# Kernel tuning notes

Measured on AMD Instinct MI355X. Metric: run time of the kernel, lower is better.

Reference implementation:

```python
import jax, jax.numpy as jnp
import numpy as np

B, IN, H = 8192, 1024, 1024
WRANK, UR0, UR1, G = 256, 64, 32, 2
HG = H // G


def setup_inputs() -> dict:
    key = jax.random.key(0)
    ks = jax.random.split(key, 24)
    r = lambda k, shp: 0.1 * jax.random.normal(k, shp, dtype=jnp.float32)
    inp = {
        "x": jax.random.normal(ks[0], (B, IN), dtype=jnp.float32),
        "h": jax.random.normal(ks[1], (B, H), dtype=jnp.float32),
        "c": jax.random.normal(ks[2], (B, H), dtype=jnp.float32),
        "W": r(ks[3], (IN, WRANK)),
        "W1": r(ks[4], (WRANK, H)),
        "W2": r(ks[5], (WRANK, H)),
        "W3": r(ks[6], (WRANK, H)),
        "W4": r(ks[7], (WRANK, H)),
        "U": r(ks[8], (G, HG, UR0)),
        "U1": r(ks[9], (G, UR0, HG)),
        "U2": r(ks[10], (G, UR0, HG)),
        "U3": r(ks[11], (G, UR0, HG)),
        "U4": r(ks[12], (G, UR0, HG)),
        "UU": r(ks[13], (G, HG, UR1)),
        "UU1": r(ks[14], (G, UR1, HG)),
        "UU2": r(ks[15], (G, UR1, HG)),
        "UU3": r(ks[16], (G, UR1, HG)),
        "UU4": r(ks[17], (G, UR1, HG)),
        "bias_f": jnp.ones((1, H), dtype=jnp.float32),
        "bias_i": jnp.ones((1, H), dtype=jnp.float32),
        "bias_c": jnp.ones((1, H), dtype=jnp.float32),
        "bias_o": jnp.ones((1, H), dtype=jnp.float32),
    }
    return inp


def _grouped(hg, Ushare, Ui):
    # hg: [B, g, hg]; Ushare: [g, hg, r]; Ui: [g, r, hg] -> [B, H]
    t = jnp.einsum('bgd,gdr->bgr', hg, Ushare)
    return jnp.einsum('bgr,grd->bgd', t, Ui).reshape(hg.shape[0], H)


def reference(x, h, c, W, W1, W2, W3, W4, U, U1, U2, U3, U4,
              UU, UU1, UU2, UU3, UU4, bias_f, bias_i, bias_c, bias_o):
    # low-rank W path
    xw = x @ W                      # [B, wRank]
    wVal1, wVal2, wVal3, wVal4 = xw @ W1, xw @ W2, xw @ W3, xw @ W4

    # grouped low-rank U path (diagonal groups)
    hg = h.reshape(B, G, HG)
    tU = jnp.einsum('bgd,gdr->bgr', hg, U)          # shared projection
    uVal1 = jnp.einsum('bgr,grd->bgd', tU, U1).reshape(B, H)
    uVal2 = jnp.einsum('bgr,grd->bgd', tU, U2).reshape(B, H)
    uVal3 = jnp.einsum('bgr,grd->bgd', tU, U3).reshape(B, H)
    uVal4 = jnp.einsum('bgr,grd->bgd', tU, U4).reshape(B, H)

    # grouped UU path on group-rotated h (index = [1..g-1, 0])
    hg3 = jnp.roll(hg, -1, axis=1)
    tUU = jnp.einsum('bgd,gdr->bgr', hg3, UU)
    uuVal1 = jnp.einsum('bgr,grd->bgd', tUU, UU1).reshape(B, H)
    uuVal2 = jnp.einsum('bgr,grd->bgd', tUU, UU2).reshape(B, H)
    uuVal3 = jnp.einsum('bgr,grd->bgd', tUU, UU3).reshape(B, H)
    uuVal4 = jnp.einsum('bgr,grd->bgd', tUU, UU4).reshape(B, H)

    matVal_i = wVal1 + uVal1 + uuVal1
    matVal_f = wVal2 + uVal2 + uuVal2
    matVal_o = wVal3 + uVal3 + uuVal3
    matVal_c = wVal4 + uVal4 + uuVal4

    i = jax.nn.sigmoid(matVal_i + bias_i)
    f = jax.nn.sigmoid(matVal_f + bias_f)
    o = jax.nn.sigmoid(matVal_o + bias_o)
    c_tilda = jnp.tanh(matVal_c + bias_c)

    c_next = f * c + i * c_tilda
    h_next = o * jnp.tanh(c_next)
    return (c_next, h_next)
```

## Files before the change

kernel.cpp:

```cpp
#include <hip/hip_runtime.h>
#include <hip/hip_bf16.h>

#define B_ROWS 8192
#define IN_DIM 1024
#define H_DIM  1024
#define WRANK  256
#define UR0    64
#define UR1    32
#define HGD    512

#define NS2    11
#define NTA    14

typedef __attribute__((ext_vector_type(8))) short bf16x8;
typedef __attribute__((ext_vector_type(4))) float f32x4;
typedef __attribute__((ext_vector_type(4))) float float4v;

__device__ __forceinline__ unsigned short f2bf(float f) {
    union { float f; unsigned u; } v; v.f = f;
    unsigned r = v.u + 0x7FFF + ((v.u >> 16) & 1);
    return (unsigned short)(r >> 16);
}

__device__ __forceinline__ void gld16(void* lds, const void* g) {
    __builtin_amdgcn_global_load_lds(
        (const __attribute__((address_space(1))) unsigned int*)g,
        (__attribute__((address_space(3))) unsigned int*)lds, 16, 0, 0);
}

__device__ __forceinline__ float fsig(float x)  { return 1.f / (1.f + __expf(-x)); }
__device__ __forceinline__ float ftanh(float x) { return 1.f - 2.f / (__expf(2.f * x) + 1.f); }

__global__ __launch_bounds__(256)
void pack_weights(const float* __restrict__ W,
                  const float* __restrict__ W1, const float* __restrict__ W2,
                  const float* __restrict__ W3, const float* __restrict__ W4,
                  const float* __restrict__ U,  const float* __restrict__ U1,
                  const float* __restrict__ U2, const float* __restrict__ U3,
                  const float* __restrict__ U4,
                  const float* __restrict__ UU, const float* __restrict__ UU1,
                  const float* __restrict__ UU2,const float* __restrict__ UU3,
                  const float* __restrict__ UU4,
                  unsigned short* __restrict__ WbfT,
                  unsigned short* __restrict__ HPbf,
                  unsigned short* __restrict__ BT2)
{
    const float* Wg[4]  = {W1, W2, W3, W4};
    const float* Ug[4]  = {U1, U2, U3, U4};
    const float* UUg[4] = {UU1, UU2, UU3, UU4};
    const long N_WT = 256L * 1024;
    const long N_HP = 256L * 512;
    const long N_BT = 16L * NS2 * 8192;
    const long total = N_WT + N_HP + N_BT;
    for (long t = blockIdx.x * 256L + threadIdx.x; t < total; t += (long)gridDim.x * 256L) {
        if (t < N_WT) {
            int n = (int)(t >> 10), p = (int)(t & 1023);
            int span = p >> 6, slp = (p >> 3) & 7, e = p & 7;
            int k = span * 64 + ((slp ^ (n & 7)) << 3) + e;
            WbfT[t] = f2bf(W[(size_t)k * WRANK + n]);
        } else if (t < N_WT + N_HP) {
            long u = t - N_WT;
            int n = (int)(u >> 9), p = (int)(u & 511);
            int span = p >> 6, slp = (p >> 3) & 7, e = p & 7;
            int k = span * 64 + ((slp ^ (n & 7)) << 3) + e;
            float v;
            if (n < 64)       v = U [(size_t)k * UR0 + n];
            else if (n < 96)  v = UU[(size_t)(HGD + k) * UR1 + (n - 64)];
            else if (n < 128) v = 0.f;
            else if (n < 192) v = U [(size_t)(HGD + k) * UR0 + (n - 128)];
            else if (n < 224) v = UU[(size_t)k * UR1 + (n - 192)];
            else              v = 0.f;
            HPbf[u] = f2bf(v);
        } else {
            long u = t - N_WT - N_HP;
            int img = (int)(u >> 13);
            int nt = img / NS2, s = img % NS2;
            int r = (int)(u & 8191);
            int q = r >> 11, kc = (r >> 9) & 3, row = (r >> 3) & 63, e = r & 7;
            int n = nt * 64 + row, g = n >> 9, nn = n & 511;
            int kk = kc * 8 + e;
            float v;
            if (s < 8)       v = Wg[q][(size_t)(s * 32 + kk) * H_DIM + n];
            else if (s < 10) v = Ug[q][((size_t)g * UR0 + (s - 8) * 32 + kk) * HGD + nn];
            else             v = UUg[q][((size_t)g * UR1 + kk) * HGD + nn];
            BT2[u] = f2bf(v);
        }
    }
}

__global__ __launch_bounds__(256, 4)
void s1_kernel(const float* __restrict__ x, const float* __restrict__ h,
               const unsigned short* __restrict__ WbfT,
               const unsigned short* __restrict__ HPbf,
               unsigned short* __restrict__ A2T)
{
    __shared__ short As[64 * 64];
    __shared__ short Bs[2][64 * 64];

    const int flat = blockIdx.x;
    const int id = (flat & 7) * 128 + (flat >> 3);
    const int bx = id & 7, by = id >> 3;
    const int m0 = by * 64;

    const bool pa = bx < 4;
    const int Kdim = pa ? IN_DIM : HGD;
    const float* Af = pa ? x : h;
    const int a_off = pa ? 0 : ((bx - 4) >> 1) * HGD;
    const unsigned short* Bw = pa ? (WbfT + (size_t)(bx * 64) * IN_DIM)
                                  : (HPbf + (size_t)((bx - 4) * 64) * HGD);
    const int ldbw = pa ? IN_DIM : HGD;
    const int ccol0 = pa ? bx * 64 : WRANK + (bx - 4) * 64;

    const int tid = threadIdx.x, lane = tid & 63, wid = tid >> 6;
    const int wr = wid >> 1, wc = wid & 1;
    const int lr = lane & 15, lh = lane >> 4;
    const int l8 = lane >> 3, l7 = lane & 7;

    f32x4 acc[2][2];
    #pragma unroll
    for (int i = 0; i < 2; ++i)
        #pragma unroll
        for (int j = 0; j < 2; ++j) acc[i][j] = (f32x4){0.f, 0.f, 0.f, 0.f};

    float4v areg[2][2][2];

#define S1_STAGEB(buf, kk) do {                                                   \
    _Pragma("unroll")                                                             \
    for (int t = 0; t < 2; ++t) {                                                 \
        int u = wid * 2 + t;                                                      \
        gld16((char*)&Bs[buf][0] + u * 1024,                                      \
              (const char*)Bw + ((size_t)(u * 8 + l8) * ldbw + (kk)) * 2 + l7 * 16); \
    } } while (0)

#define S1_LOADA(set, kk) do {                                                    \
    _Pragma("unroll")                                                             \
    for (int t = 0; t < 2; ++t) {                                                 \
        int cc = tid + t * 256;                                                   \
        int row = cc >> 3, slot = cc & 7;                                         \
        const float* p = Af + (size_t)(m0 + row) * 1024 + a_off + (kk) + slot * 8;\
        areg[set][t][0] = *(const float4v*)p;                                     \
        areg[set][t][1] = *(const float4v*)(p + 4);                               \
    } } while (0)

#define S1_WRITEA(set) do {                                                       \
    _Pragma("unroll")                                                             \
    for (int t = 0; t < 2; ++t) {                                                 \
        int cc = tid + t * 256;                                                   \
        int row = cc >> 3, slot = cc & 7;                                         \
        union { bf16x8 v; unsigned short s_[8]; } uv;                             \
        uv.s_[0] = f2bf(areg[set][t][0].x); uv.s_[1] = f2bf(areg[set][t][0].y);   \
        uv.s_[2] = f2bf(areg[set][t][0].z); uv.s_[3] = f2bf(areg[set][t][0].w);   \
        uv.s_[4] = f2bf(areg[set][t][1].x); uv.s_[5] = f2bf(areg[set][t][1].y);   \
        uv.s_[6] = f2bf(areg[set][t][1].z); uv.s_[7] = f2bf(areg[set][t][1].w);   \
        *(bf16x8*)((char*)As + row * 128 + ((slot ^ (row & 7)) << 4)) = uv.v;     \
    } } while (0)

    S1_STAGEB(0, 0);
    S1_LOADA(0, 0);

    #pragma unroll
    for (int ki = 0; ki < 16; ++ki) {
        if (ki * 64 >= Kdim) break;
        const int cur = ki & 1;
        const bool more = (ki + 1) * 64 < Kdim;
        if (more) S1_STAGEB(cur ^ 1, (ki + 1) * 64);
        if (more) { asm volatile("s_waitcnt vmcnt(2)" ::: "memory"); }
        else      { asm volatile("s_waitcnt vmcnt(0)" ::: "memory"); }
        S1_WRITEA(cur);
        if (more) S1_LOADA(cur ^ 1, (ki + 1) * 64);
        asm volatile("s_waitcnt lgkmcnt(0)" ::: "memory");
        __builtin_amdgcn_s_barrier();
        asm volatile("" ::: "memory");
        #pragma unroll
        for (int ks = 0; ks < 2; ++ks) {
            bf16x8 af[2];
            #pragma unroll
            for (int i = 0; i < 2; ++i) {
                int r = wr * 32 + i * 16 + lr;
                af[i] = *(const bf16x8*)((const char*)As + r * 128
                        + (((ks * 4 + lh) ^ (r & 7)) << 4));
            }
            #pragma unroll
            for (int j = 0; j < 2; ++j) {
                int r = wc * 32 + j * 16 + lr;
                bf16x8 rb = *(const bf16x8*)((const char*)&Bs[cur][0] + r * 128
                            + (((ks * 4 + lh) ^ (r & 7)) << 4));
                #pragma unroll
                for (int i = 0; i < 2; ++i)
                    acc[i][j] = __builtin_amdgcn_mfma_f32_16x16x32_bf16(
                        af[i], rb, acc[i][j], 0, 0, 0);
            }
        }
        asm volatile("" ::: "memory");
        __builtin_amdgcn_s_barrier();
        asm volatile("" ::: "memory");
    }
#undef S1_STAGEB
#undef S1_LOADA
#undef S1_WRITEA

    #pragma unroll
    for (int i = 0; i < 2; ++i) {
        #pragma unroll
        for (int j = 0; j < 2; ++j) {
            int ncol = ccol0 + wc * 32 + j * 16 + lr;
            int blk = ncol >> 5;
            if (blk == 11 || blk == 15) continue;
            int tt = (blk <= 10) ? blk : blk - 1;
            int kk = ncol & 31, kc = kk >> 3, e = kk & 7;
            #pragma unroll
            for (int rr = 0; rr < 4; ++rr) {
                int brow = m0 + wr * 32 + i * 16 + lh * 4 + rr;
                A2T[((size_t)(brow >> 8) * NTA + tt) * 8192 + kc * 2048
                    + (brow & 255) * 8 + e] = f2bf(acc[i][j][rr]);
            }
        }
    }
}

__global__ __launch_bounds__(512, 4)
void s2_kernel(const unsigned short* __restrict__ A2T,
               const unsigned short* __restrict__ BT2,
               const float* __restrict__ bias_f, const float* __restrict__ bias_i,
               const float* __restrict__ bias_c, const float* __restrict__ bias_o,
               const float* __restrict__ cin,
               float* __restrict__ cout, float* __restrict__ hout)
{
    __shared__ short As[2][128 * 32];
    __shared__ short Bs[2][4 * 64 * 32];

    const int flat = blockIdx.x;
    const int id = (flat & 7) * 128 + (flat >> 3);
    const int nt = id & 15, mt = id >> 4;
    const int m0 = mt * 128, n0 = nt * 64, g = nt >> 3;

    const int tid = threadIdx.x, lane = tid & 63, wid = tid >> 6;
    const int wr = wid >> 2, wc = wid & 3;
    const int lr = lane & 15, lh = lane >> 4;

    const char* Abase = (const char*)A2T + (size_t)(mt >> 1) * NTA * 16384
                        + (mt & 1) * 2048 + (wid >> 1) * 4096 + (wid & 1) * 1024
                        + lane * 16;
    const char* Bbase = (const char*)BT2 + (size_t)nt * NS2 * 16384 + lane * 16;

    f32x4 acc[4][4];
    #pragma unroll
    for (int q = 0; q < 4; ++q)
        #pragma unroll
        for (int i = 0; i < 4; ++i) acc[q][i] = (f32x4){0.f, 0.f, 0.f, 0.f};

#define S2_TA(s) ((s) < 8 ? (s) : (g == 0 ? ((s) == 10 ? 13 : (s)) \
                                          : ((s) == 10 ? 10 : (s) + 3)))
#define S2_STAGE(buf, s, tA) do {                                                 \
    gld16((char*)&As[buf][0] + wid * 1024, Abase + (size_t)(tA) * 16384);         \
    _Pragma("unroll")                                                             \
    for (int t = 0; t < 2; ++t) {                                                 \
        int u = wid * 2 + t;                                                      \
        gld16((char*)&Bs[buf][0] + u * 1024,                                      \
              Bbase + (size_t)(s) * 16384 + u * 1024);                            \
    } } while (0)

    S2_STAGE(0, 0, 0);

    #pragma unroll
    for (int s = 0; s < NS2; ++s) {
        const int cur = s & 1;
        if (s < NS2 - 1) {
            const int sn = s + 1;
            const int tA = S2_TA(sn);
            S2_STAGE(cur ^ 1, sn, tA);
            asm volatile("s_waitcnt vmcnt(3)" ::: "memory");
        } else {
            asm volatile("s_waitcnt vmcnt(0)" ::: "memory");
        }
        __builtin_amdgcn_s_barrier();
        asm volatile("" ::: "memory");
        __builtin_amdgcn_s_setprio(1);
        {
            bf16x8 af[4];
            #pragma unroll
            for (int i = 0; i < 4; ++i)
                af[i] = *(const bf16x8*)((const char*)&As[cur][0]
                        + lh * 2048 + (wr * 64 + i * 16 + lr) * 16);
            #pragma unroll
            for (int q = 0; q < 4; ++q) {
                bf16x8 rb = *(const bf16x8*)((const char*)&Bs[cur][0]
                            + q * 4096 + lh * 1024 + (wc * 16 + lr) * 16);
                #pragma unroll
                for (int i = 0; i < 4; ++i)
                    acc[q][i] = __builtin_amdgcn_mfma_f32_16x16x32_bf16(
                        af[i], rb, acc[q][i], 0, 0, 0);
            }
        }
        __builtin_amdgcn_s_setprio(0);
        asm volatile("" ::: "memory");
        __builtin_amdgcn_s_barrier();
        asm volatile("" ::: "memory");
    }
#undef S2_STAGE
#undef S2_TA

    const int ncol = n0 + wc * 16 + lr;
    const float Bi = bias_i[ncol], Bf = bias_f[ncol];
    const float Bo = bias_o[ncol], Bc = bias_c[ncol];
    #pragma unroll
    for (int i = 0; i < 4; ++i) {
        #pragma unroll
        for (int rr = 0; rr < 4; ++rr) {
            int brow = m0 + wr * 64 + i * 16 + lh * 4 + rr;
            float mi = acc[0][i][rr] + Bi;
            float mf = acc[1][i][rr] + Bf;
            float mo = acc[2][i][rr] + Bo;
            float mc = acc[3][i][rr] + Bc;
            float iv = fsig(mi), fv = fsig(mf), ov = fsig(mo);
            float ct = ftanh(mc);
            float cv = cin[(size_t)brow * H_DIM + ncol];
            float cn = fv * cv + iv * ct;
            float hn = ov * ftanh(cn);
            cout[(size_t)brow * H_DIM + ncol] = cn;
            hout[(size_t)brow * H_DIM + ncol] = hn;
        }
    }
}

extern "C" void kernel_launch(void* const* d_in, const int* in_sizes, int n_in,
                              void* d_out, int out_size, void* d_ws, size_t ws_size,
                              hipStream_t stream)
{
    const float* x   = (const float*)d_in[0];
    const float* h   = (const float*)d_in[1];
    const float* c   = (const float*)d_in[2];
    const float* W   = (const float*)d_in[3];
    const float* W1  = (const float*)d_in[4];
    const float* W2  = (const float*)d_in[5];
    const float* W3  = (const float*)d_in[6];
    const float* W4  = (const float*)d_in[7];
    const float* U   = (const float*)d_in[8];
    const float* U1  = (const float*)d_in[9];
    const float* U2  = (const float*)d_in[10];
    const float* U3  = (const float*)d_in[11];
    const float* U4  = (const float*)d_in[12];
    const float* UU  = (const float*)d_in[13];
    const float* UU1 = (const float*)d_in[14];
    const float* UU2 = (const float*)d_in[15];
    const float* UU3 = (const float*)d_in[16];
    const float* UU4 = (const float*)d_in[17];
    const float* bias_f = (const float*)d_in[18];
    const float* bias_i = (const float*)d_in[19];
    const float* bias_c = (const float*)d_in[20];
    const float* bias_o = (const float*)d_in[21];

    unsigned short* A2T  = (unsigned short*)d_ws;
    unsigned short* WbfT = A2T  + 32L * NTA * 8192;
    unsigned short* HPbf = WbfT + 256L * 1024;
    unsigned short* BT2  = HPbf + 256L * 512;

    float* c_out = (float*)d_out;
    float* h_out = c_out + (size_t)B_ROWS * H_DIM;

    pack_weights<<<dim3(2048), dim3(256), 0, stream>>>(
        W, W1, W2, W3, W4, U, U1, U2, U3, U4, UU, UU1, UU2, UU3, UU4,
        WbfT, HPbf, BT2);

    s1_kernel<<<dim3(1024), dim3(256), 0, stream>>>(x, h, WbfT, HPbf, A2T);

    s2_kernel<<<dim3(1024), dim3(512), 0, stream>>>(
        A2T, BT2, bias_f, bias_i, bias_c, bias_o, c, c_out, h_out);
}
```

Before: 84.22 us.

## Triple-buffer both GEMM stages and prefetch cell state during the main loop

Both kernels move from double to triple buffering, so global-to-LDS loads are issued two K-steps ahead and the vmcnt waits are retuned to match. In the second kernel the cell-state input c is loaded into registers partway through the K loop, so the epilogue no longer stalls on that global read. In exchange, LDS use and register pressure go up, which may lower occupancy. The hand-counted vmcnt values also have to be exact, or the kernels will read stale data.

```diff
diff --git a/kernel.cpp b/kernel.cpp
--- a/kernel.cpp
+++ b/kernel.cpp
@@ -95,7 +95,7 @@
                unsigned short* __restrict__ A2T)
 {
     __shared__ short As[64 * 64];
-    __shared__ short Bs[2][64 * 64];
+    __shared__ short Bs[3][64 * 64];
 
     const int flat = blockIdx.x;
     const int id = (flat & 7) * 128 + (flat >> 3);
@@ -122,17 +122,15 @@
         #pragma unroll
         for (int j = 0; j < 2; ++j) acc[i][j] = (f32x4){0.f, 0.f, 0.f, 0.f};
 
-    float4v areg[2][2][2];
-
-#define S1_STAGEB(buf, kk) do {                                                   \
+    float4v areg[3][2][2];
+
+#define S1_ISSUE(set, kk) do {                                                    \
     _Pragma("unroll")                                                             \
     for (int t = 0; t < 2; ++t) {                                                 \
         int u = wid * 2 + t;                                                      \
-        gld16((char*)&Bs[buf][0] + u * 1024,                                      \
+        gld16((char*)&Bs[set][0] + u * 1024,                                      \
               (const char*)Bw + ((size_t)(u * 8 + l8) * ldbw + (kk)) * 2 + l7 * 16); \
-    } } while (0)
-
-#define S1_LOADA(set, kk) do {                                                    \
+    }                                                                             \
     _Pragma("unroll")                                                             \
     for (int t = 0; t < 2; ++t) {                                                 \
         int cc = tid + t * 256;                                                   \
@@ -155,48 +153,52 @@
         *(bf16x8*)((char*)As + row * 128 + ((slot ^ (row & 7)) << 4)) = uv.v;     \
     } } while (0)
 
-    S1_STAGEB(0, 0);
-    S1_LOADA(0, 0);
+    S1_ISSUE(0, 0);
+    S1_ISSUE(1, 64);
 
     #pragma unroll
     for (int ki = 0; ki < 16; ++ki) {
         if (ki * 64 >= Kdim) break;
-        const int cur = ki & 1;
-        const bool more = (ki + 1) * 64 < Kdim;
-        if (more) S1_STAGEB(cur ^ 1, (ki + 1) * 64);
-        if (more) { asm volatile("s_waitcnt vmcnt(2)" ::: "memory"); }
-        else      { asm volatile("s_waitcnt vmcnt(0)" ::: "memory"); }
-        S1_WRITEA(cur);
-        if (more) S1_LOADA(cur ^ 1, (ki + 1) * 64);
+        const bool issue = (ki + 2) * 64 < Kdim;
+        if (issue) {
+            const int set = (ki + 2) % 3;
+            S1_ISSUE(set, (ki + 2) * 64);
+        }
+        if (issue)                          { asm volatile("s_waitcnt vmcnt(12)" ::: "memory"); }
+        else if ((ki + 1) * 64 < Kdim)      { asm volatile("s_waitcnt vmcnt(6)"  ::: "memory"); }
+        else                                { asm volatile("s_waitcnt vmcnt(0)"  ::: "memory"); }
+        S1_WRITEA(ki % 3);
         asm volatile("s_waitcnt lgkmcnt(0)" ::: "memory");
         __builtin_amdgcn_s_barrier();
         asm volatile("" ::: "memory");
-        #pragma unroll
-        for (int ks = 0; ks < 2; ++ks) {
-            bf16x8 af[2];
-            #pragma unroll
-            for (int i = 0; i < 2; ++i) {
-                int r = wr * 32 + i * 16 + lr;
-                af[i] = *(const bf16x8*)((const char*)As + r * 128
-                        + (((ks * 4 + lh) ^ (r & 7)) << 4));
+        {
+            const int cur = ki % 3;
+            #pragma unroll
+            for (int ks = 0; ks < 2; ++ks) {
+                bf16x8 af[2];
+                #pragma unroll
+                for (int i = 0; i < 2; ++i) {
+                    int r = wr * 32 + i * 16 + lr;
+                    af[i] = *(const bf16x8*)((const char*)As + r * 128
+                            + (((ks * 4 + lh) ^ (r & 7)) << 4));
+                }
+                #pragma unroll
+                for (int j = 0; j < 2; ++j) {
+                    int r = wc * 32 + j * 16 + lr;
+                    bf16x8 rb = *(const bf16x8*)((const char*)&Bs[cur][0] + r * 128
+                                + (((ks * 4 + lh) ^ (r & 7)) << 4));
+                    #pragma unroll
+                    for (int i = 0; i < 2; ++i)
+                        acc[i][j] = __builtin_amdgcn_mfma_f32_16x16x32_bf16(
+                            af[i], rb, acc[i][j], 0, 0, 0);
+                }
             }
-            #pragma unroll
-            for (int j = 0; j < 2; ++j) {
-                int r = wc * 32 + j * 16 + lr;
-                bf16x8 rb = *(const bf16x8*)((const char*)&Bs[cur][0] + r * 128
-                            + (((ks * 4 + lh) ^ (r & 7)) << 4));
-                #pragma unroll
-                for (int i = 0; i < 2; ++i)
-                    acc[i][j] = __builtin_amdgcn_mfma_f32_16x16x32_bf16(
-                        af[i], rb, acc[i][j], 0, 0, 0);
-            }
         }
         asm volatile("" ::: "memory");
         __builtin_amdgcn_s_barrier();
         asm volatile("" ::: "memory");
     }
-#undef S1_STAGEB
-#undef S1_LOADA
+#undef S1_ISSUE
 #undef S1_WRITEA
 
     #pragma unroll
@@ -226,8 +228,8 @@
                const float* __restrict__ cin,
                float* __restrict__ cout, float* __restrict__ hout)
 {
-    __shared__ short As[2][128 * 32];
-    __shared__ short Bs[2][4 * 64 * 32];
+    __shared__ short As[3][128 * 32];
+    __shared__ short Bs[3][4 * 64 * 32];
 
     const int flat = blockIdx.x;
     const int id = (flat & 7) * 128 + (flat >> 3);
@@ -242,12 +244,15 @@
                         + (mt & 1) * 2048 + (wid >> 1) * 4096 + (wid & 1) * 1024
                         + lane * 16;
     const char* Bbase = (const char*)BT2 + (size_t)nt * NS2 * 16384 + lane * 16;
+    const int ncol = n0 + wc * 16 + lr;
 
     f32x4 acc[4][4];
     #pragma unroll
     for (int q = 0; q < 4; ++q)
         #pragma unroll
         for (int i = 0; i < 4; ++i) acc[q][i] = (f32x4){0.f, 0.f, 0.f, 0.f};
+
+    float cv[4][4];
 
 #define S2_TA(s) ((s) < 8 ? (s) : (g == 0 ? ((s) == 10 ? 13 : (s)) \
                                           : ((s) == 10 ? 10 : (s) + 3)))
@@ -261,18 +266,30 @@
     } } while (0)
 
     S2_STAGE(0, 0, 0);
+    S2_STAGE(1, 1, 1);
 
     #pragma unroll
     for (int s = 0; s < NS2; ++s) {
-        const int cur = s & 1;
-        if (s < NS2 - 1) {
-            const int sn = s + 1;
+        const int cur = s % 3;
+        if (s + 2 < NS2) {
+            const int sn = s + 2;
             const int tA = S2_TA(sn);
-            S2_STAGE(cur ^ 1, sn, tA);
-            asm volatile("s_waitcnt vmcnt(3)" ::: "memory");
-        } else {
-            asm volatile("s_waitcnt vmcnt(0)" ::: "memory");
-        }
+            S2_STAGE(sn % 3, sn, tA);
+        }
+        if (s == 8) {
+            asm volatile("" ::: "memory");
+            #pragma unroll
+            for (int i = 0; i < 4; ++i)
+                #pragma unroll
+                for (int rr = 0; rr < 4; ++rr)
+                    cv[i][rr] = cin[(size_t)(m0 + wr * 64 + i * 16 + lh * 4 + rr)
+                                    * H_DIM + ncol];
+            asm volatile("" ::: "memory");
+        }
+        if (s < 8)       { asm volatile("s_waitcnt vmcnt(6)"  ::: "memory"); }
+        else if (s == 8) { asm volatile("s_waitcnt vmcnt(22)" ::: "memory"); }
+        else if (s == 9) { asm volatile("s_waitcnt vmcnt(19)" ::: "memory"); }
+        else             { asm volatile("s_waitcnt vmcnt(16)" ::: "memory"); }
         __builtin_amdgcn_s_barrier();
         asm volatile("" ::: "memory");
         __builtin_amdgcn_s_setprio(1);
@@ -300,7 +317,6 @@
 #undef S2_STAGE
 #undef S2_TA
 
-    const int ncol = n0 + wc * 16 + lr;
     const float Bi = bias_i[ncol], Bf = bias_f[ncol];
     const float Bo = bias_o[ncol], Bc = bias_c[ncol];
     #pragma unroll
@@ -314,8 +330,7 @@
             float mc = acc[3][i][rr] + Bc;
             float iv = fsig(mi), fv = fsig(mf), ov = fsig(mo);
             float ct = ftanh(mc);
-            float cv = cin[(size_t)brow * H_DIM + ncol];
-            float cn = fv * cv + iv * ct;
+            float cn = fv * cv[i][rr] + iv * ct;
             float hn = ov * ftanh(cn);
             cout[(size_t)brow * H_DIM + ncol] = cn;
             hout[(size_t)brow * H_DIM + ncol] = hn;
```

Measured after the change: 175.3 us. 108% more time.

## Triple-buffer s2 LDS stages, swap tile raster order, split MFMA phases

Applied to the files above, without the earlier changes.

The s2 GEMM+LSTM kernel moves from double to triple buffering, prefetching two stages ahead (vmcnt 6), so global loads have more time to land before compute. Block-to-tile mapping changes so consecutive blocks walk M within one N tile, which changes L2 reuse of the B operand. The MFMA inner loop is split into two halves separated by an extra barrier, with B fragments loaded up front and A fragments loaded per half. In exchange the kernel uses more LDS (which may lower occupancy) and adds a barrier per stage.

```diff
diff --git a/kernel.cpp b/kernel.cpp
--- a/kernel.cpp
+++ b/kernel.cpp
@@ -226,12 +226,12 @@
                const float* __restrict__ cin,
                float* __restrict__ cout, float* __restrict__ hout)
 {
-    __shared__ short As[2][128 * 32];
-    __shared__ short Bs[2][4 * 64 * 32];
+    __shared__ short As[3][4 * 128 * 8];
+    __shared__ short Bs[3][4 * 4 * 64 * 8];
 
     const int flat = blockIdx.x;
     const int id = (flat & 7) * 128 + (flat >> 3);
-    const int nt = id & 15, mt = id >> 4;
+    const int nt = id >> 6, mt = id & 63;
     const int m0 = mt * 128, n0 = nt * 64, g = nt >> 3;
 
     const int tid = threadIdx.x, lane = tid & 63, wid = tid >> 6;
@@ -239,7 +239,7 @@
     const int lr = lane & 15, lh = lane >> 4;
 
     const char* Abase = (const char*)A2T + (size_t)(mt >> 1) * NTA * 16384
-                        + (mt & 1) * 2048 + (wid >> 1) * 4096 + (wid & 1) * 1024
+                        + (wid >> 1) * 4096 + (mt & 1) * 2048 + (wid & 1) * 1024
                         + lane * 16;
     const char* Bbase = (const char*)BT2 + (size_t)nt * NS2 * 16384 + lane * 16;
 
@@ -255,44 +255,63 @@
     gld16((char*)&As[buf][0] + wid * 1024, Abase + (size_t)(tA) * 16384);         \
     _Pragma("unroll")                                                             \
     for (int t = 0; t < 2; ++t) {                                                 \
-        int u = wid * 2 + t;                                                      \
-        gld16((char*)&Bs[buf][0] + u * 1024,                                      \
-              Bbase + (size_t)(s) * 16384 + u * 1024);                            \
+        int v = wid * 2 + t;                                                      \
+        gld16((char*)&Bs[buf][0] + v * 1024,                                      \
+              Bbase + (size_t)(s) * 16384 + v * 1024);                            \
     } } while (0)
 
     S2_STAGE(0, 0, 0);
+    S2_STAGE(1, 1, 1);
 
     #pragma unroll
     for (int s = 0; s < NS2; ++s) {
-        const int cur = s & 1;
-        if (s < NS2 - 1) {
-            const int sn = s + 1;
-            const int tA = S2_TA(sn);
-            S2_STAGE(cur ^ 1, sn, tA);
+        const int cur = s % 3;
+        if (s + 2 < NS2) {
+            S2_STAGE((s + 2) % 3, s + 2, S2_TA(s + 2));
+            asm volatile("s_waitcnt vmcnt(6)" ::: "memory");
+        } else if (s + 1 < NS2) {
             asm volatile("s_waitcnt vmcnt(3)" ::: "memory");
         } else {
             asm volatile("s_waitcnt vmcnt(0)" ::: "memory");
         }
         __builtin_amdgcn_s_barrier();
         asm volatile("" ::: "memory");
-        __builtin_amdgcn_s_setprio(1);
+
+        bf16x8 rb[4];
+        #pragma unroll
+        for (int q = 0; q < 4; ++q)
+            rb[q] = *(const bf16x8*)((const char*)&Bs[cur][0]
+                    + q * 4096 + lh * 1024 + (wc * 16 + lr) * 16);
         {
-            bf16x8 af[4];
-            #pragma unroll
-            for (int i = 0; i < 4; ++i)
-                af[i] = *(const bf16x8*)((const char*)&As[cur][0]
-                        + lh * 2048 + (wr * 64 + i * 16 + lr) * 16);
+            bf16x8 af0 = *(const bf16x8*)((const char*)&As[cur][0]
+                         + lh * 2048 + (wr * 64 + 0 * 16 + lr) * 16);
+            bf16x8 af1 = *(const bf16x8*)((const char*)&As[cur][0]
+                         + lh * 2048 + (wr * 64 + 1 * 16 + lr) * 16);
+            __builtin_amdgcn_s_setprio(1);
             #pragma unroll
             for (int q = 0; q < 4; ++q) {
-                bf16x8 rb = *(const bf16x8*)((const char*)&Bs[cur][0]
-                            + q * 4096 + lh * 1024 + (wc * 16 + lr) * 16);
-                #pragma unroll
-                for (int i = 0; i < 4; ++i)
-                    acc[q][i] = __builtin_amdgcn_mfma_f32_16x16x32_bf16(
-                        af[i], rb, acc[q][i], 0, 0, 0);
-            }
-        }
-        __builtin_amdgcn_s_setprio(0);
+                acc[q][0] = __builtin_amdgcn_mfma_f32_16x16x32_bf16(af0, rb[q], acc[q][0], 0, 0, 0);
+                acc[q][1] = __builtin_amdgcn_mfma_f32_16x16x32_bf16(af1, rb[q], acc[q][1], 0, 0, 0);
+            }
+            __builtin_amdgcn_s_setprio(0);
+        }
+        asm volatile("" ::: "memory");
+        __builtin_amdgcn_s_barrier();
+        asm volatile("" ::: "memory");
+
+        {
+            bf16x8 af2 = *(const bf16x8*)((const char*)&As[cur][0]
+                         + lh * 2048 + (wr * 64 + 2 * 16 + lr) * 16);
+            bf16x8 af3 = *(const bf16x8*)((const char*)&As[cur][0]
+                         + lh * 2048 + (wr * 64 + 3 * 16 + lr) * 16);
+            __builtin_amdgcn_s_setprio(1);
+            #pragma unroll
+            for (int q = 0; q < 4; ++q) {
+                acc[q][2] = __builtin_amdgcn_mfma_f32_16x16x32_bf16(af2, rb[q], acc[q][2], 0, 0, 0);
+                acc[q][3] = __builtin_amdgcn_mfma_f32_16x16x32_bf16(af3, rb[q], acc[q][3], 0, 0, 0);
+            }
+            __builtin_amdgcn_s_setprio(0);
+        }
         asm volatile("" ::: "memory");
         __builtin_amdgcn_s_barrier();
         asm volatile("" ::: "memory");
```

Result: no change. 83.24 us (-1.2%).
